# Kernel tuning notes

Hardware: AMD Instinct MI355X
Metric: run time of the kernel (lower is better)

The kernel has to match this reference:

```python
import jax, jax.numpy as jnp
import numpy as np

EMBED = 2048
N_HEAD = 32
N_KV = 8
HEAD_DIM = 64
GROUP = N_HEAD // N_KV


def _rope_tables(seq_len, head_dim):
    inv_freq = 1.0 / (10000.0 ** (jnp.arange(0, head_dim, 2, dtype=jnp.float32) / head_dim))
    ang = jnp.arange(seq_len, dtype=jnp.float32)[:, None] * inv_freq[None, :]  # [S, D/2]
    ang = jnp.concatenate([ang, ang], axis=-1)  # [S, D]
    return jnp.cos(ang), jnp.sin(ang)


def apply_rope(x, cos, sin, offset=0):
    # x: [B, H, S, D]
    S, D = x.shape[2], x.shape[3]
    x1, x2 = x[..., : D // 2], x[..., D // 2 :]
    c = cos[offset : offset + S][None, None]
    s = sin[offset : offset + S][None, None]
    rotated = jnp.concatenate([-x2, x1], axis=-1)
    return (x * c + rotated * s).astype(x.dtype)


def setup_inputs() -> dict:
    key = jax.random.key(0)
    kx, kq, kk, kv, ko = jax.random.split(key, 5)
    B, S = 2, 2048
    x = jax.random.normal(kx, (B, S, EMBED), dtype=jnp.float32)
    mask = jnp.triu(jnp.ones((S, S), dtype=bool), k=1)  # causal: True = masked
    cos, sin = _rope_tables(S, HEAD_DIM)
    std = 0.02
    Wq = jax.random.normal(kq, (EMBED, EMBED), dtype=jnp.float32) * std
    Wk = jax.random.normal(kk, (EMBED, N_KV * HEAD_DIM), dtype=jnp.float32) * std
    Wv = jax.random.normal(kv, (EMBED, N_KV * HEAD_DIM), dtype=jnp.float32) * std
    Wo = jax.random.normal(ko, (EMBED, EMBED), dtype=jnp.float32) * std
    return {"x": x, "mask": mask, "cos": cos, "sin": sin,
            "Wq": Wq, "Wk": Wk, "Wv": Wv, "Wo": Wo}


def reference(x, mask, cos, sin, Wq, Wk, Wv, Wo):
    B, S, E = x.shape
    # projections (no bias)
    q = (x @ Wq).reshape(B, S, N_HEAD, HEAD_DIM).transpose(0, 2, 1, 3)  # [B,H,S,D]
    k = (x @ Wk).reshape(B, S, N_KV, HEAD_DIM).transpose(0, 2, 1, 3)    # [B,G,S,D]
    v = (x @ Wv).reshape(B, S, N_KV, HEAD_DIM).transpose(0, 2, 1, 3)    # [B,G,S,D]
    q = apply_rope(q, cos, sin, offset=0)
    k = apply_rope(k, cos, sin, offset=0)
    next_k, next_v = k, v  # kv cache to return
    # GQA: head h uses kv group h // GROUP; avoid repeat_interleave via reshape
    qg = q.reshape(B, N_KV, GROUP, S, HEAD_DIM)
    scores = jnp.einsum('bgjsd,bgtd->bgjst', qg, k) / np.float32(np.sqrt(HEAD_DIM))
    scores = jnp.where(mask[None, None, None], -jnp.inf, scores)
    attn = jax.nn.softmax(scores, axis=-1)
    out = jnp.einsum('bgjst,bgtd->bgjsd', attn, v)          # [B,G,group,S,D]
    out = out.reshape(B, N_HEAD, S, HEAD_DIM).transpose(0, 2, 1, 3).reshape(B, S, E)
    return out @ Wo, next_k, next_v
```

## Files before the change

### kernel.cpp

```cpp
#include <hip/hip_runtime.h>
#include <hip/hip_bf16.h>
#include <math.h>

#define NH 32
#define NKV 8
#define HD 64
#define B_ 2
#define S_ 2048
#define E_ 2048
#define M_ 4096

typedef unsigned short ushort_t;
typedef __attribute__((ext_vector_type(8))) short short8;
typedef __attribute__((ext_vector_type(4))) short short4v;
typedef __attribute__((ext_vector_type(4))) float floatx4;

__device__ inline unsigned short f2bf(float f) {
  unsigned int u = __float_as_uint(f);
  return (unsigned short)((u + 0x7FFFu + ((u >> 16) & 1u)) >> 16);
}

__device__ inline float fexp2(float x) {
  float r;
  asm("v_exp_f32 %0, %1" : "=v"(r) : "v"(x));
  return r;
}

__device__ inline void ld_lds16(const void* g, void* l) {
  __builtin_amdgcn_global_load_lds((__attribute__((address_space(1))) void*)g,
                                   (__attribute__((address_space(3))) void*)l, 16, 0, 0);
}

__device__ inline void transp32(const float* __restrict__ in, ushort_t* __restrict__ out,
                                int R, int C, int bx, int by, int tid, float (*tile)[33]) {
  int c0 = bx * 32, r0 = by * 32;
  int x = tid & 31, y0 = tid >> 5;
  for (int i = 0; i < 4; i++) {
    int r = y0 + i * 8;
    tile[r][x] = in[(size_t)(r0 + r) * C + c0 + x];
  }
  __syncthreads();
  for (int i = 0; i < 4; i++) {
    int r = y0 + i * 8;
    out[(size_t)(c0 + r) * R + r0 + x] = f2bf(tile[x][r]);
  }
}

__global__ __launch_bounds__(256) void prep(const float* __restrict__ x,
                                            ushort_t* __restrict__ xb,
                                            const float* __restrict__ Wq,
                                            const float* __restrict__ Wk,
                                            const float* __restrict__ Wv,
                                            const float* __restrict__ Wo,
                                            ushort_t* __restrict__ WT,
                                            ushort_t* __restrict__ WoT) {
  __shared__ float tile[32][33];
  int bid = blockIdx.x, tid = threadIdx.x;
  if (bid < 4096) {
    size_t i = ((size_t)bid * 256 + tid) * 8;
    float4 a = *(const float4*)(x + i);
    float4 b = *(const float4*)(x + i + 4);
    short8 o;
    o[0] = (short)f2bf(a.x); o[1] = (short)f2bf(a.y);
    o[2] = (short)f2bf(a.z); o[3] = (short)f2bf(a.w);
    o[4] = (short)f2bf(b.x); o[5] = (short)f2bf(b.y);
    o[6] = (short)f2bf(b.z); o[7] = (short)f2bf(b.w);
    *(short8*)(xb + i) = o;
    return;
  }
  bid -= 4096;
  if (bid < 4096) { transp32(Wq, WT, 2048, 2048, bid & 63, bid >> 6, tid, tile); return; }
  bid -= 4096;
  if (bid < 1024) { transp32(Wk, WT + 2048 * 2048, 2048, 512, bid & 15, bid >> 4, tid, tile); return; }
  bid -= 1024;
  if (bid < 1024) { transp32(Wv, WT + 2560 * 2048, 2048, 512, bid & 15, bid >> 4, tid, tile); return; }
  bid -= 1024;
  transp32(Wo, WoT, 2048, 2048, bid & 63, bid >> 6, tid, tile);
}

__global__ __launch_bounds__(512) void gemm_qkv(const ushort_t* __restrict__ xb,
                                                const ushort_t* __restrict__ WT,
                                                ushort_t* __restrict__ qbf,
                                                float* __restrict__ outk,
                                                ushort_t* __restrict__ kbf,
                                                float* __restrict__ outv,
                                                ushort_t* __restrict__ vt,
                                                const float* __restrict__ cosP,
                                                const float* __restrict__ sinP) {
  __shared__ __align__(16) ushort_t L8[2][2][2][128][64];
  char* Lb = (char*)L8;
  int bid = blockIdx.x;
  int xcd = bid & 7, ii = bid >> 3;
  int mg = xcd >> 1, ng = xcd & 1;
  int m0 = (mg * 4 + ii / 6) * 256;
  int n0 = (ng * 6 + ii % 6) * 256;
  int tid = threadIdx.x;
  int w8 = tid >> 6, lane = tid & 63;
  int wrq = w8 >> 1, wcq = w8 & 1;
  int lr = lane & 15, quad = lane >> 4;
  int sx = lr & 7;
  int srow = w8 * 16 + (lane >> 3);
  int schunk = (lane & 7) ^ (lane >> 3);
  const char* abase = (const char*)(xb + (size_t)m0 * 2048);
  const char* bbase = (const char*)(WT + (size_t)n0 * 2048);
  floatx4 acc[4][2][4] = {};

#define STG(T, U)                                                                        \
  do {                                                                                   \
    const int mat_ = (U)&1, half_ = (U) >> 1;                                            \
    const char* sp = (mat_ ? bbase : abase) + (size_t)(half_ * 128 + srow) * 4096 +      \
                     (size_t)(T)*128 + schunk * 16;                                      \
    char* dp = Lb + (((T)&1) * 65536) + mat_ * 32768 + half_ * 16384 + w8 * 2048;        \
    ld_lds16(sp, dp);                                                                    \
    ld_lds16(sp + (size_t)8 * 4096, dp + 1024);                                          \
  } while (0)

#define PH(T, P, MH_, NH_, WAITS, DOSTAGE)                                               \
  do {                                                                                   \
    asm volatile(WAITS ::: "memory");                                                    \
    const char* Ab_ = Lb + (((T)&1) * 65536) + (MH_)*16384;                              \
    const char* Bb_ = Lb + (((T)&1) * 65536) + 32768 + (NH_)*16384;                      \
    short8 af_[2][2], bf_[4][2];                                                         \
    _Pragma("unroll") for (int i = 0; i < 2; i++) {                                      \
      size_t rb = (size_t)(wrq * 32 + i * 16 + lr) * 128;                                \
      _Pragma("unroll") for (int ks = 0; ks < 2; ks++)                                   \
          af_[i][ks] = *(const short8*)(Ab_ + rb + (((ks * 4 + quad) ^ sx) << 4));       \
    }                                                                                    \
    _Pragma("unroll") for (int j = 0; j < 4; j++) {                                      \
      size_t rb = (size_t)(wcq * 64 + j * 16 + lr) * 128;                                \
      _Pragma("unroll") for (int ks = 0; ks < 2; ks++)                                   \
          bf_[j][ks] = *(const short8*)(Bb_ + rb + (((ks * 4 + quad) ^ sx) << 4));       \
    }                                                                                    \
    if (DOSTAGE) STG((T) + 1, P);                                                        \
    __builtin_amdgcn_s_setprio(1);                                                       \
    _Pragma("unroll") for (int i = 0; i < 2; i++) _Pragma("unroll") for (int j = 0;      \
                                                                         j < 4; j++) {  \
      acc[P][i][j] =                                                                     \
          __builtin_amdgcn_mfma_f32_16x16x32_bf16(af_[i][0], bf_[j][0], acc[P][i][j],    \
                                                  0, 0, 0);                              \
      acc[P][i][j] =                                                                     \
          __builtin_amdgcn_mfma_f32_16x16x32_bf16(af_[i][1], bf_[j][1], acc[P][i][j],    \
                                                  0, 0, 0);                              \
    }                                                                                    \
    __builtin_amdgcn_s_setprio(0);                                                       \
  } while (0)

  STG(0, 0); STG(0, 1); STG(0, 2); STG(0, 3);

  for (int kt = 0; kt < 31; kt++) {
    PH(kt, 0, 0, 0, "s_waitcnt vmcnt(4)\n\ts_barrier", 1);
    PH(kt, 1, 1, 0, "s_waitcnt vmcnt(4)\n\ts_barrier", 1);
    PH(kt, 2, 1, 1, "s_waitcnt vmcnt(4)\n\ts_barrier", 1);
    PH(kt, 3, 0, 1, "s_barrier", 1);
  }
  PH(31, 0, 0, 0, "s_waitcnt vmcnt(4)\n\ts_barrier", 0);
  PH(31, 1, 1, 0, "s_waitcnt vmcnt(2)\n\ts_barrier", 0);
  PH(31, 2, 1, 1, "s_waitcnt vmcnt(0)\n\ts_barrier", 0);
  PH(31, 3, 0, 1, "s_barrier", 0);
#undef STG
#undef PH

  const int MHs[4] = {0, 1, 1, 0}, NHs[4] = {0, 0, 1, 1};
  if (n0 < 2048) {
    const float QS = 0.125f * 1.4426950408889634f;
#pragma unroll
    for (int p = 0; p < 4; p++)
#pragma unroll
      for (int i = 0; i < 2; i++)
#pragma unroll
        for (int j = 0; j < 2; j++) {
          int d = j * 16 + lr;
#pragma unroll
          for (int r = 0; r < 4; r++) {
            int row = m0 + MHs[p] * 128 + wrq * 32 + i * 16 + quad * 4 + r;
            int s = row & (S_ - 1);
            float c = cosP[s * 64 + d], sn = sinP[s * 64 + d];
            float x1 = acc[p][i][j][r], x2 = acc[p][i][j + 2][r];
            size_t oo = (size_t)row * 2048 + n0 + NHs[p] * 128 + wcq * 64 + d;
            qbf[oo] = f2bf((x1 * c - x2 * sn) * QS);
            qbf[oo + 32] = f2bf((x2 * c + x1 * sn) * QS);
          }
        }
  } else if (n0 < 2560) {
#pragma unroll
    for (int p = 0; p < 4; p++) {
      int h = ((n0 - 2048) >> 6) + NHs[p] * 2 + wcq;
#pragma unroll
      for (int i = 0; i < 2; i++)
#pragma unroll
        for (int j = 0; j < 2; j++) {
          int d = j * 16 + lr;
#pragma unroll
          for (int r = 0; r < 4; r++) {
            int row = m0 + MHs[p] * 128 + wrq * 32 + i * 16 + quad * 4 + r;
            int s = row & (S_ - 1), b = row >> 11;
            float c = cosP[s * 64 + d], sn = sinP[s * 64 + d];
            float x1 = acc[p][i][j][r], x2 = acc[p][i][j + 2][r];
            float y1 = x1 * c - x2 * sn, y2 = x2 * c + x1 * sn;
            size_t rowb = ((size_t)(b * NKV + h) * S_ + s) * 64;
            int xr = (s & 7) << 3;
            outk[rowb + d] = y1; outk[rowb + d + 32] = y2;
            kbf[rowb + (d ^ xr)] = f2bf(y1);
            kbf[rowb + ((d + 32) ^ xr)] = f2bf(y2);
          }
        }
    }
  } else {
#pragma unroll
    for (int p = 0; p < 4; p++) {
      int h = ((n0 - 2560) >> 6) + NHs[p] * 2 + wcq;
#pragma unroll
      for (int i = 0; i < 2; i++)
#pragma unroll
        for (int j = 0; j < 4; j++) {
          int d = j * 16 + lr;
          int row0 = m0 + MHs[p] * 128 + wrq * 32 + i * 16 + quad * 4;
          int s0 = row0 & (S_ - 1), b = row0 >> 11;
#pragma unroll
          for (int r = 0; r < 4; r++)
            outv[((size_t)(b * NKV + h) * S_ + s0 + r) * 64 + d] = acc[p][i][j][r];
          int tt = s0 >> 6, s4 = s0 & 63;
          short4v u;
          u[0] = (short)f2bf(acc[p][i][j][0]); u[1] = (short)f2bf(acc[p][i][j][1]);
          u[2] = (short)f2bf(acc[p][i][j][2]); u[3] = (short)f2bf(acc[p][i][j][3]);
          *(short4v*)(vt + ((size_t)(b * NKV + h) * 32 + tt) * 4096 + d * 64 +
                      (s4 ^ ((d & 7) << 3))) = u;
        }
    }
  }
}

__device__ __forceinline__ void gemm128_core(const ushort_t* __restrict__ Ag,
                                             const ushort_t* __restrict__ Bg,
                                             floatx4 (&acc)[4][4]) {
  __shared__ __align__(16) ushort_t As[2][128][64];
  __shared__ __align__(16) ushort_t Bs[2][128][64];
  int tid = threadIdx.x;
  int w = tid >> 6, lane = tid & 63;
  int wm = (w >> 1) * 64, wn = (w & 1) * 64;
  int lr = lane & 15, quad = lane >> 4;
  int sx = lr & 7;
  char* Asb = (char*)As;
  char* Bsb = (char*)Bs;

  size_t so[4];
#pragma unroll
  for (int s = 0; s < 4; s++)
    so[s] = (size_t)(w * 32 + s * 8 + (lane >> 3)) * 4096 + (size_t)(((lane & 7) ^ (lane >> 3)) * 16);
  const char* abase = (const char*)Ag;
  const char* bbase = (const char*)Bg;

#define STAGE128(buf, kt)                                          \
  do {                                                             \
    size_t ko = (size_t)(kt) * 128;                                \
    char* Ad = Asb + (buf) * 16384 + w * 4096;                     \
    char* Bd = Bsb + (buf) * 16384 + w * 4096;                     \
    _Pragma("unroll") for (int s = 0; s < 4; s++) {                \
      ld_lds16(abase + so[s] + ko, Ad + s * 1024);                 \
      ld_lds16(bbase + so[s] + ko, Bd + s * 1024);                 \
    }                                                              \
  } while (0)

  STAGE128(0, 0);
  __syncthreads();

  int cur = 0;
  for (int kt = 0; kt < 32; kt++) {
    if (kt < 31) STAGE128(cur ^ 1, kt + 1);
    const char* Ab = Asb + cur * 16384;
    const char* Bb = Bsb + cur * 16384;
    short8 af[4][2], bfr[4][2];
#pragma unroll
    for (int i = 0; i < 4; i++) {
      size_t rb = (size_t)(wm + i * 16 + lr) * 128;
#pragma unroll
      for (int ks = 0; ks < 2; ks++)
        af[i][ks] = *(const short8*)(Ab + rb + (((ks * 4 + quad) ^ sx) << 4));
    }
#pragma unroll
    for (int j = 0; j < 4; j++) {
      size_t rb = (size_t)(wn + j * 16 + lr) * 128;
#pragma unroll
      for (int ks = 0; ks < 2; ks++)
        bfr[j][ks] = *(const short8*)(Bb + rb + (((ks * 4 + quad) ^ sx) << 4));
    }
#pragma unroll
    for (int i = 0; i < 4; i++)
#pragma unroll
      for (int j = 0; j < 4; j++) {
        acc[i][j] = __builtin_amdgcn_mfma_f32_16x16x32_bf16(af[i][0], bfr[j][0], acc[i][j], 0, 0, 0);
        acc[i][j] = __builtin_amdgcn_mfma_f32_16x16x32_bf16(af[i][1], bfr[j][1], acc[i][j], 0, 0, 0);
      }
    __syncthreads();
    cur ^= 1;
  }
#undef STAGE128
}

__global__ __launch_bounds__(256) void gemm_o(const ushort_t* __restrict__ ctx,
                                              const ushort_t* __restrict__ WoT,
                                              float* __restrict__ y) {
  int o = blockIdx.y * 16 + blockIdx.x;
  int xcd = o & 7, i = o >> 3;
  int mg = xcd >> 1, ng = xcd & 1;
  int m0 = (mg * 8 + (i >> 3)) * 128;
  int n0 = (ng * 8 + (i & 7)) * 128;
  int tid = threadIdx.x;
  int w = tid >> 6, lane = tid & 63;
  int wm = (w >> 1) * 64, wn = (w & 1) * 64;
  int lr = lane & 15, quad = lane >> 4;

  floatx4 acc[4][4] = {};
  gemm128_core(ctx + (size_t)m0 * 2048, WoT + (size_t)n0 * 2048, acc);

#pragma unroll
  for (int i2 = 0; i2 < 4; i2++)
#pragma unroll
    for (int j = 0; j < 4; j++) {
      int row = m0 + wm + i2 * 16 + quad * 4;
      int col = n0 + wn + j * 16 + lr;
#pragma unroll
      for (int r = 0; r < 4; r++)
        y[(size_t)(row + r) * 2048 + col] = acc[i2][j][r];
    }
}

__global__ __launch_bounds__(256, 4) void attn2(ushort_t* __restrict__ q,
                                                const ushort_t* __restrict__ k,
                                                const ushort_t* __restrict__ vt) {
  __shared__ __align__(16) ushort_t KV[2][2][64][64];
  __shared__ __align__(16) ushort_t Ps[4][16][64];
  int bh = blockIdx.x;
  int qt = 31 - blockIdx.y;
  int b = bh >> 5, h = bh & 31, g = h >> 2;
  int tid = threadIdx.x;
  int w = tid >> 6, lane = tid & 63;
  int lr = lane & 15, quad = lane >> 4;

  int qg = qt * 64 + w * 16 + lr;
  short8 aq0, aq1;
  {
    const ushort_t* qp = q + ((size_t)(b * S_ + qg) * NH + h) * HD;
    aq0 = *(const short8*)(qp + quad * 8);
    aq1 = *(const short8*)(qp + 32 + quad * 8);
  }
  floatx4 od[4] = {};
  float mi = -INFINITY, li = 0.f;

  const char* ksrc = (const char*)(k + (size_t)(b * NKV + g) * S_ * HD) + w * 2048 + lane * 16;
  const char* vsrc = (const char*)(vt + (size_t)(b * NKV + g) * S_ * HD) + w * 2048 + lane * 16;
  char* dB = (char*)&KV[0][0][0][0] + w * 2048;

  int sw = (lr & 7) << 4;
  int ro0 = (quad * 16) ^ sw;
  int ro1 = (64 + quad * 16) ^ sw;
  char* Pw = (char*)&Ps[0][0][0] + w * 2048;

  ld_lds16(ksrc, dB);
  ld_lds16(ksrc + 1024, dB + 1024);
  ld_lds16(vsrc, dB + 8192);
  ld_lds16(vsrc + 1024, dB + 8192 + 1024);
  asm volatile("s_waitcnt vmcnt(0)" ::: "memory");
  __syncthreads();

  int cur = 0;
  for (int t = 0; t <= qt; t++) {
    if (t < qt) {
      const char* kn = ksrc + (size_t)(t + 1) * 8192;
      const char* vn = vsrc + (size_t)(t + 1) * 8192;
      char* d = dB + (cur ^ 1) * 16384;
      ld_lds16(kn, d); ld_lds16(kn + 1024, d + 1024);
      ld_lds16(vn, d + 8192); ld_lds16(vn + 1024, d + 8192 + 1024);
    }
    const char* Kb = (const char*)&KV[cur][0][0][0];
    const char* Vb = (const char*)&KV[cur][1][0][0];
    floatx4 sc[4];
    __builtin_amdgcn_s_setprio(1);
#pragma unroll
    for (int kn = 0; kn < 4; kn++) {
      short8 a0 = *(const short8*)(Kb + (kn * 16 + lr) * 128 + ro0);
      short8 a1 = *(const short8*)(Kb + (kn * 16 + lr) * 128 + ro1);
      floatx4 c = {};
      c = __builtin_amdgcn_mfma_f32_16x16x32_bf16(a0, aq0, c, 0, 0, 0);
      c = __builtin_amdgcn_mfma_f32_16x16x32_bf16(a1, aq1, c, 0, 0, 0);
      sc[kn] = c;
    }
    __builtin_amdgcn_s_setprio(0);
    float pv[16];
#pragma unroll
    for (int kn = 0; kn < 4; kn++)
#pragma unroll
      for (int r = 0; r < 4; r++) pv[kn * 4 + r] = sc[kn][r];
    if (t == qt) {
#pragma unroll
      for (int e = 0; e < 16; e++) {
        int kg = t * 64 + (e >> 2) * 16 + quad * 4 + (e & 3);
        if (kg > qg) pv[e] = -INFINITY;
      }
    }
    float mx = pv[0];
#pragma unroll
    for (int e = 1; e < 16; e++) mx = fmaxf(mx, pv[e]);
    mx = fmaxf(mx, __shfl_xor(mx, 16));
    mx = fmaxf(mx, __shfl_xor(mx, 32));
    if (__any(mx > mi + 11.5f)) {
      float mn = fmaxf(mi, mx);
      float al = fexp2(mi - mn);
      li *= al;
#pragma unroll
      for (int dn = 0; dn < 4; dn++) {
        od[dn][0] *= al; od[dn][1] *= al; od[dn][2] *= al; od[dn][3] *= al;
      }
      mi = mn;
    }
    float ps = 0.f;
#pragma unroll
    for (int e = 0; e < 16; e++) {
      pv[e] = fexp2(pv[e] - mi);
      ps += pv[e];
    }
    ps += __shfl_xor(ps, 16);
    ps += __shfl_xor(ps, 32);
    li += ps;
#pragma unroll
    for (int kn = 0; kn < 4; kn++) {
      unsigned int u0, u1;
      asm("v_cvt_pk_bf16_f32 %0, %1, %2" : "=v"(u0) : "v"(pv[kn * 4 + 0]), "v"(pv[kn * 4 + 1]));
      asm("v_cvt_pk_bf16_f32 %0, %1, %2" : "=v"(u1) : "v"(pv[kn * 4 + 2]), "v"(pv[kn * 4 + 3]));
      uint2 uu; uu.x = u0; uu.y = u1;
      *(uint2*)(Pw + lr * 128 + ((kn * 32 + quad * 8) ^ sw)) = uu;
    }
    short8 pb0 = *(const short8*)(Pw + lr * 128 + ro0);
    short8 pb1 = *(const short8*)(Pw + lr * 128 + ro1);
    __builtin_amdgcn_s_setprio(1);
#pragma unroll
    for (int dn = 0; dn < 4; dn++) {
      short8 va = *(const short8*)(Vb + (dn * 16 + lr) * 128 + ro0);
      short8 vb = *(const short8*)(Vb + (dn * 16 + lr) * 128 + ro1);
      od[dn] = __builtin_amdgcn_mfma_f32_16x16x32_bf16(va, pb0, od[dn], 0, 0, 0);
      od[dn] = __builtin_amdgcn_mfma_f32_16x16x32_bf16(vb, pb1, od[dn], 0, 0, 0);
    }
    __builtin_amdgcn_s_setprio(0);
    asm volatile("s_waitcnt vmcnt(0)" ::: "memory");
    __syncthreads();
    cur ^= 1;
  }
  float inv = 1.f / li;
  ushort_t* outp = q + ((size_t)(b * S_ + qg) * NH + h) * HD;
#pragma unroll
  for (int dn = 0; dn < 4; dn++) {
    short4v u;
    u[0] = (short)f2bf(od[dn][0] * inv); u[1] = (short)f2bf(od[dn][1] * inv);
    u[2] = (short)f2bf(od[dn][2] * inv); u[3] = (short)f2bf(od[dn][3] * inv);
    *(short4v*)(outp + dn * 16 + quad * 4) = u;
  }
}

extern "C" void kernel_launch(void* const* d_in, const int* in_sizes, int n_in,
                              void* d_out, int out_size, void* d_ws, size_t ws_size,
                              hipStream_t stream) {
  const float* x = (const float*)d_in[0];
  const float* cosT = (const float*)d_in[2];
  const float* sinT = (const float*)d_in[3];
  const float* Wq = (const float*)d_in[4];
  const float* Wk = (const float*)d_in[5];
  const float* Wv = (const float*)d_in[6];
  const float* Wo = (const float*)d_in[7];

  char* ws = (char*)d_ws;
  ushort_t* WT = (ushort_t*)(ws);
  ushort_t* WoT = (ushort_t*)(ws + 12582912);
  ushort_t* xb = (ushort_t*)(ws + 20971520);
  ushort_t* qbf = (ushort_t*)(ws + 37748736);
  ushort_t* kbf = (ushort_t*)(ws + 54525952);
  ushort_t* vt = (ushort_t*)(ws + 58720256);

  float* y = (float*)d_out;
  float* outk = y + (size_t)M_ * E_;
  float* outv = outk + (size_t)B_ * NKV * S_ * HD;

  prep<<<dim3(14336), 256, 0, stream>>>(x, xb, Wq, Wk, Wv, Wo, WT, WoT);

  gemm_qkv<<<dim3(192), 512, 0, stream>>>(xb, WT, qbf, outk, kbf, outv, vt, cosT, sinT);

  attn2<<<dim3(64, 32), 256, 0, stream>>>(qbf, kbf, vt);

  gemm_o<<<dim3(16, 32), 256, 0, stream>>>(qbf, WoT, y);
}
```

Measured before the change: 308.6 us.

## Process two 64-row query tiles per attention block to reuse K/V tiles

Measured after the change: 303.9 us. About the same (-1.5%).

```diff
diff --git a/kernel.cpp b/kernel.cpp
--- a/kernel.cpp
+++ b/kernel.cpp
@@ -325,27 +325,31 @@
     }
 }
 
-__global__ __launch_bounds__(256, 4) void attn2(ushort_t* __restrict__ q,
+__global__ __launch_bounds__(256, 3) void attn2(ushort_t* __restrict__ q,
                                                 const ushort_t* __restrict__ k,
                                                 const ushort_t* __restrict__ vt) {
   __shared__ __align__(16) ushort_t KV[2][2][64][64];
-  __shared__ __align__(16) ushort_t Ps[4][16][64];
+  __shared__ __align__(16) ushort_t Ps[4][2][16][64];
   int bh = blockIdx.x;
-  int qt = 31 - blockIdx.y;
+  int qi = 15 - blockIdx.y;
   int b = bh >> 5, h = bh & 31, g = h >> 2;
   int tid = threadIdx.x;
   int w = tid >> 6, lane = tid & 63;
   int lr = lane & 15, quad = lane >> 4;
 
-  int qg = qt * 64 + w * 16 + lr;
-  short8 aq0, aq1;
+  int qg0 = qi * 128 + w * 16 + lr;
+  int qg1 = qg0 + 64;
+  short8 a00, a01, a10, a11;
   {
-    const ushort_t* qp = q + ((size_t)(b * S_ + qg) * NH + h) * HD;
-    aq0 = *(const short8*)(qp + quad * 8);
-    aq1 = *(const short8*)(qp + 32 + quad * 8);
-  }
-  floatx4 od[4] = {};
-  float mi = -INFINITY, li = 0.f;
+    const ushort_t* qp0 = q + ((size_t)(b * S_ + qg0) * NH + h) * HD;
+    const ushort_t* qp1 = q + ((size_t)(b * S_ + qg1) * NH + h) * HD;
+    a00 = *(const short8*)(qp0 + quad * 8);
+    a01 = *(const short8*)(qp0 + 32 + quad * 8);
+    a10 = *(const short8*)(qp1 + quad * 8);
+    a11 = *(const short8*)(qp1 + 32 + quad * 8);
+  }
+  floatx4 od0[4] = {}, od1[4] = {};
+  float mi0 = -INFINITY, li0 = 0.f, mi1 = -INFINITY, li1 = 0.f;
 
   const char* ksrc = (const char*)(k + (size_t)(b * NKV + g) * S_ * HD) + w * 2048 + lane * 16;
   const char* vsrc = (const char*)(vt + (size_t)(b * NKV + g) * S_ * HD) + w * 2048 + lane * 16;
@@ -354,7 +358,7 @@
   int sw = (lr & 7) << 4;
   int ro0 = (quad * 16) ^ sw;
   int ro1 = (64 + quad * 16) ^ sw;
-  char* Pw = (char*)&Ps[0][0][0] + w * 2048;
+  char* Pw = (char*)&Ps[0][0][0][0] + w * 4096;
 
   ld_lds16(ksrc, dB);
   ld_lds16(ksrc + 1024, dB + 1024);
@@ -363,9 +367,10 @@
   asm volatile("s_waitcnt vmcnt(0)" ::: "memory");
   __syncthreads();
 
+  int T = 2 * qi + 2;
   int cur = 0;
-  for (int t = 0; t <= qt; t++) {
-    if (t < qt) {
+  for (int t = 0; t < T; t++) {
+    if (t + 1 < T) {
       const char* kn = ksrc + (size_t)(t + 1) * 8192;
       const char* vn = vsrc + (size_t)(t + 1) * 8192;
       char* d = dB + (cur ^ 1) * 16384;
@@ -374,85 +379,165 @@
     }
     const char* Kb = (const char*)&KV[cur][0][0][0];
     const char* Vb = (const char*)&KV[cur][1][0][0];
-    floatx4 sc[4];
+    bool dq0 = (t == 2 * qi);
+    bool skip0 = (t == 2 * qi + 1);
+    if (!skip0) {
+      floatx4 sc[4];
+      __builtin_amdgcn_s_setprio(1);
+#pragma unroll
+      for (int kn = 0; kn < 4; kn++) {
+        short8 k0 = *(const short8*)(Kb + (kn * 16 + lr) * 128 + ro0);
+        short8 k1 = *(const short8*)(Kb + (kn * 16 + lr) * 128 + ro1);
+        floatx4 c = {};
+        c = __builtin_amdgcn_mfma_f32_16x16x32_bf16(k0, a00, c, 0, 0, 0);
+        c = __builtin_amdgcn_mfma_f32_16x16x32_bf16(k1, a01, c, 0, 0, 0);
+        sc[kn] = c;
+      }
+      __builtin_amdgcn_s_setprio(0);
+      float pv[16];
+#pragma unroll
+      for (int kn = 0; kn < 4; kn++)
+#pragma unroll
+        for (int r = 0; r < 4; r++) pv[kn * 4 + r] = sc[kn][r];
+      if (dq0) {
+#pragma unroll
+        for (int e = 0; e < 16; e++) {
+          int kg = t * 64 + (e >> 2) * 16 + quad * 4 + (e & 3);
+          if (kg > qg0) pv[e] = -INFINITY;
+        }
+      }
+      float mx = pv[0];
+#pragma unroll
+      for (int e = 1; e < 16; e++) mx = fmaxf(mx, pv[e]);
+      mx = fmaxf(mx, __shfl_xor(mx, 16));
+      mx = fmaxf(mx, __shfl_xor(mx, 32));
+      if (__any(mx > mi0 + 11.5f)) {
+        float mn = fmaxf(mi0, mx);
+        float al = fexp2(mi0 - mn);
+        li0 *= al;
+#pragma unroll
+        for (int dn = 0; dn < 4; dn++) {
+          od0[dn][0] *= al; od0[dn][1] *= al; od0[dn][2] *= al; od0[dn][3] *= al;
+        }
+        mi0 = mn;
+      }
+      float ps = 0.f;
+#pragma unroll
+      for (int e = 0; e < 16; e++) {
+        pv[e] = fexp2(pv[e] - mi0);
+        ps += pv[e];
+      }
+      ps += __shfl_xor(ps, 16);
+      ps += __shfl_xor(ps, 32);
+      li0 += ps;
+#pragma unroll
+      for (int kn = 0; kn < 4; kn++) {
+        unsigned int u0, u1;
+        asm("v_cvt_pk_bf16_f32 %0, %1, %2" : "=v"(u0) : "v"(pv[kn * 4 + 0]), "v"(pv[kn * 4 + 1]));
+        asm("v_cvt_pk_bf16_f32 %0, %1, %2" : "=v"(u1) : "v"(pv[kn * 4 + 2]), "v"(pv[kn * 4 + 3]));
+        uint2 uu; uu.x = u0; uu.y = u1;
+        *(uint2*)(Pw + lr * 128 + ((kn * 32 + quad * 8) ^ sw)) = uu;
+      }
+    }
+    {
+      floatx4 sc[4];
+      __builtin_amdgcn_s_setprio(1);
+#pragma unroll
+      for (int kn = 0; kn < 4; kn++) {
+        short8 k0 = *(const short8*)(Kb + (kn * 16 + lr) * 128 + ro0);
+        short8 k1 = *(const short8*)(Kb + (kn * 16 + lr) * 128 + ro1);
+        floatx4 c = {};
+        c = __builtin_amdgcn_mfma_f32_16x16x32_bf16(k0, a10, c, 0, 0, 0);
+        c = __builtin_amdgcn_mfma_f32_16x16x32_bf16(k1, a11, c, 0, 0, 0);
+        sc[kn] = c;
+      }
+      __builtin_amdgcn_s_setprio(0);
+      float pv[16];
+#pragma unroll
+      for (int kn = 0; kn < 4; kn++)
+#pragma unroll
+        for (int r = 0; r < 4; r++) pv[kn * 4 + r] = sc[kn][r];
+      if (skip0) {
+#pragma unroll
+        for (int e = 0; e < 16; e++) {
+          int kg = t * 64 + (e >> 2) * 16 + quad * 4 + (e & 3);
+          if (kg > qg1) pv[e] = -INFINITY;
+        }
+      }
+      float mx = pv[0];
+#pragma unroll
+      for (int e = 1; e < 16; e++) mx = fmaxf(mx, pv[e]);
+      mx = fmaxf(mx, __shfl_xor(mx, 16));
+      mx = fmaxf(mx, __shfl_xor(mx, 32));
+      if (__any(mx > mi1 + 11.5f)) {
+        float mn = fmaxf(mi1, mx);
+        float al = fexp2(mi1 - mn);
+        li1 *= al;
+#pragma unroll
+        for (int dn = 0; dn < 4; dn++) {
+          od1[dn][0] *= al; od1[dn][1] *= al; od1[dn][2] *= al; od1[dn][3] *= al;
+        }
+        mi1 = mn;
+      }
+      float ps = 0.f;
+#pragma unroll
+      for (int e = 0; e < 16; e++) {
+        pv[e] = fexp2(pv[e] - mi1);
+        ps += pv[e];
+      }
+      ps += __shfl_xor(ps, 16);
+      ps += __shfl_xor(ps, 32);
+      li1 += ps;
+#pragma unroll
+      for (int kn = 0; kn < 4; kn++) {
+        unsigned int u0, u1;
+        asm("v_cvt_pk_bf16_f32 %0, %1, %2" : "=v"(u0) : "v"(pv[kn * 4 + 0]), "v"(pv[kn * 4 + 1]));
+        asm("v_cvt_pk_bf16_f32 %0, %1, %2" : "=v"(u1) : "v"(pv[kn * 4 + 2]), "v"(pv[kn * 4 + 3]));
+        uint2 uu; uu.x = u0; uu.y = u1;
+        *(uint2*)(Pw + 2048 + lr * 128 + ((kn * 32 + quad * 8) ^ sw)) = uu;
+      }
+    }
     __builtin_amdgcn_s_setprio(1);
-#pragma unroll
-    for (int kn = 0; kn < 4; kn++) {
-      short8 a0 = *(const short8*)(Kb + (kn * 16 + lr) * 128 + ro0);
-      short8 a1 = *(const short8*)(Kb + (kn * 16 + lr) * 128 + ro1);
-      floatx4 c = {};
-      c = __builtin_amdgcn_mfma_f32_16x16x32_bf16(a0, aq0, c, 0, 0, 0);
-      c = __builtin_amdgcn_mfma_f32_16x16x32_bf16(a1, aq1, c, 0, 0, 0);
-      sc[kn] = c;
-    }
-    __builtin_amdgcn_s_setprio(0);
-    float pv[16];
-#pragma unroll
-    for (int kn = 0; kn < 4; kn++)
-#pragma unroll
-      for (int r = 0; r < 4; r++) pv[kn * 4 + r] = sc[kn][r];
-    if (t == qt) {
-#pragma unroll
-      for (int e = 0; e < 16; e++) {
-        int kg = t * 64 + (e >> 2) * 16 + quad * 4 + (e & 3);
-        if (kg > qg) pv[e] = -INFINITY;
-      }
-    }
-    float mx = pv[0];
-#pragma unroll
-    for (int e = 1; e < 16; e++) mx = fmaxf(mx, pv[e]);
-    mx = fmaxf(mx, __shfl_xor(mx, 16));
-    mx = fmaxf(mx, __shfl_xor(mx, 32));
-    if (__any(mx > mi + 11.5f)) {
-      float mn = fmaxf(mi, mx);
-      float al = fexp2(mi - mn);
-      li *= al;
+    if (!skip0) {
+      short8 pb0 = *(const short8*)(Pw + lr * 128 + ro0);
+      short8 pb1 = *(const short8*)(Pw + lr * 128 + ro1);
 #pragma unroll
       for (int dn = 0; dn < 4; dn++) {
-        od[dn][0] *= al; od[dn][1] *= al; od[dn][2] *= al; od[dn][3] *= al;
-      }
-      mi = mn;
-    }
-    float ps = 0.f;
-#pragma unroll
-    for (int e = 0; e < 16; e++) {
-      pv[e] = fexp2(pv[e] - mi);
-      ps += pv[e];
-    }
-    ps += __shfl_xor(ps, 16);
-    ps += __shfl_xor(ps, 32);
-    li += ps;
-#pragma unroll
-    for (int kn = 0; kn < 4; kn++) {
-      unsigned int u0, u1;
-      asm("v_cvt_pk_bf16_f32 %0, %1, %2" : "=v"(u0) : "v"(pv[kn * 4 + 0]), "v"(pv[kn * 4 + 1]));
-      asm("v_cvt_pk_bf16_f32 %0, %1, %2" : "=v"(u1) : "v"(pv[kn * 4 + 2]), "v"(pv[kn * 4 + 3]));
-      uint2 uu; uu.x = u0; uu.y = u1;
-      *(uint2*)(Pw + lr * 128 + ((kn * 32 + quad * 8) ^ sw)) = uu;
-    }
-    short8 pb0 = *(const short8*)(Pw + lr * 128 + ro0);
-    short8 pb1 = *(const short8*)(Pw + lr * 128 + ro1);
-    __builtin_amdgcn_s_setprio(1);
-#pragma unroll
-    for (int dn = 0; dn < 4; dn++) {
-      short8 va = *(const short8*)(Vb + (dn * 16 + lr) * 128 + ro0);
-      short8 vb = *(const short8*)(Vb + (dn * 16 + lr) * 128 + ro1);
-      od[dn] = __builtin_amdgcn_mfma_f32_16x16x32_bf16(va, pb0, od[dn], 0, 0, 0);
-      od[dn] = __builtin_amdgcn_mfma_f32_16x16x32_bf16(vb, pb1, od[dn], 0, 0, 0);
+        short8 va = *(const short8*)(Vb + (dn * 16 + lr) * 128 + ro0);
+        short8 vb = *(const short8*)(Vb + (dn * 16 + lr) * 128 + ro1);
+        od0[dn] = __builtin_amdgcn_mfma_f32_16x16x32_bf16(va, pb0, od0[dn], 0, 0, 0);
+        od0[dn] = __builtin_amdgcn_mfma_f32_16x16x32_bf16(vb, pb1, od0[dn], 0, 0, 0);
+      }
+    }
+    {
+      short8 pb0 = *(const short8*)(Pw + 2048 + lr * 128 + ro0);
+      short8 pb1 = *(const short8*)(Pw + 2048 + lr * 128 + ro1);
+#pragma unroll
+      for (int dn = 0; dn < 4; dn++) {
+        short8 va = *(const short8*)(Vb + (dn * 16 + lr) * 128 + ro0);
+        short8 vb = *(const short8*)(Vb + (dn * 16 + lr) * 128 + ro1);
+        od1[dn] = __builtin_amdgcn_mfma_f32_16x16x32_bf16(va, pb0, od1[dn], 0, 0, 0);
+        od1[dn] = __builtin_amdgcn_mfma_f32_16x16x32_bf16(vb, pb1, od1[dn], 0, 0, 0);
+      }
     }
     __builtin_amdgcn_s_setprio(0);
     asm volatile("s_waitcnt vmcnt(0)" ::: "memory");
     __syncthreads();
     cur ^= 1;
   }
-  float inv = 1.f / li;
-  ushort_t* outp = q + ((size_t)(b * S_ + qg) * NH + h) * HD;
+  float inv0 = 1.f / li0, inv1 = 1.f / li1;
+  ushort_t* outp0 = q + ((size_t)(b * S_ + qg0) * NH + h) * HD;
+  ushort_t* outp1 = q + ((size_t)(b * S_ + qg1) * NH + h) * HD;
 #pragma unroll
   for (int dn = 0; dn < 4; dn++) {
     short4v u;
-    u[0] = (short)f2bf(od[dn][0] * inv); u[1] = (short)f2bf(od[dn][1] * inv);
-    u[2] = (short)f2bf(od[dn][2] * inv); u[3] = (short)f2bf(od[dn][3] * inv);
-    *(short4v*)(outp + dn * 16 + quad * 4) = u;
+    u[0] = (short)f2bf(od0[dn][0] * inv0); u[1] = (short)f2bf(od0[dn][1] * inv0);
+    u[2] = (short)f2bf(od0[dn][2] * inv0); u[3] = (short)f2bf(od0[dn][3] * inv0);
+    *(short4v*)(outp0 + dn * 16 + quad * 4) = u;
+    short4v v;
+    v[0] = (short)f2bf(od1[dn][0] * inv1); v[1] = (short)f2bf(od1[dn][1] * inv1);
+    v[2] = (short)f2bf(od1[dn][2] * inv1); v[3] = (short)f2bf(od1[dn][3] * inv1);
+    *(short4v*)(outp1 + dn * 16 + quad * 4) = v;
   }
 }
 
@@ -483,7 +568,7 @@
 
   gemm_qkv<<<dim3(192), 512, 0, stream>>>(xb, WT, qbf, outk, kbf, outv, vt, cosT, sinT);
 
-  attn2<<<dim3(64, 32), 256, 0, stream>>>(qbf, kbf, vt);
+  attn2<<<dim3(64, 16), 256, 0, stream>>>(qbf, kbf, vt);
 
   gemm_o<<<dim3(16, 32), 256, 0, stream>>>(qbf, WoT, y);
 }
```
